# Performance work log

Measured on AMD Instinct MI355X. Metric: run time of the kernel, lower is better.

## Reference

```python
import jax, jax.numpy as jnp
import numpy as np

BN_EPS = 1e-5

def _vq(x, embed):
    # x: (..., dim), embed: (dim, K). Nearest-codeword lookup with straight-through.
    dim = x.shape[-1]
    flat = x.reshape(-1, dim)
    dist = (flat * flat).sum(1, keepdims=True) - 2.0 * (flat @ embed) + (embed * embed).sum(0, keepdims=True)
    ids = jnp.argmin(dist, axis=1)
    q = jnp.take(embed.T, ids, axis=0).reshape(x.shape)
    diff = jnp.mean((jax.lax.stop_gradient(q) - x) ** 2)
    q = x + jax.lax.stop_gradient(q - x)
    return q, diff

def _weight_quantize(W, embed, in_mem, out_mem):
    # W: (out_f, in_f). Group W.T into (out_g, in_g, in_mem*out_mem) blocks,
    # VQ each block, scatter back to (out_f, in_f). Matches torch chunk/stack loops.
    out_f, in_f = W.shape
    in_g, out_g = in_f // in_mem, out_f // out_mem
    g = W.T.reshape(in_g, in_mem, out_g, out_mem).transpose(2, 0, 1, 3).reshape(out_g, in_g, in_mem * out_mem)
    q, diff = _vq(g, embed)
    qW = q.reshape(out_g, in_g, in_mem, out_mem).transpose(0, 3, 1, 2).reshape(out_f, in_f)
    return qW, diff

def _bn(x, gamma, beta):
    # training-mode BatchNorm1d: biased batch variance
    mu = x.mean(axis=0)
    var = ((x - mu) ** 2).mean(axis=0)
    return (x - mu) * jax.lax.rsqrt(var + BN_EPS) * gamma + beta


def setup_inputs() -> dict:
    key = jax.random.key(0)
    ks = jax.random.split(key, 8)
    B, D_IN, H, D_OUT, K = 65536, 784, 512, 10, 512
    s = 0.05
    return {
        "x": jax.random.normal(ks[0], (B, D_IN), jnp.float32),
        "W1": jax.random.normal(ks[1], (H, D_IN), jnp.float32) * s,
        "b1": jnp.zeros((H,), jnp.float32),
        "gamma1": jnp.ones((H,), jnp.float32),
        "beta1": jnp.zeros((H,), jnp.float32),
        "E1": jax.random.normal(ks[2], (28, K), jnp.float32) * s,  # dim = in_mem(7)*out_mem(4)
        "W2": jax.random.normal(ks[3], (H, H), jnp.float32) * s,
        "b2": jnp.zeros((H,), jnp.float32),
        "E2": jax.random.normal(ks[4], (16, K), jnp.float32) * s,  # dim = in_mem(16)*out_mem(1)
        "W3": jax.random.normal(ks[5], (D_OUT, H), jnp.float32) * s,
        "b3": jnp.zeros((D_OUT,), jnp.float32),
    }


def reference(x, W1, b1, gamma1, beta1, E1, W2, b2, E2, W3, b3):
    qW1, diff1 = _weight_quantize(W1, E1, 7, 4)
    h = jax.nn.relu(x @ qW1.T + b1)
    qW2, diff2 = _weight_quantize(W2, E2, 16, 1)
    h = jax.nn.relu(_bn(h, gamma1, beta1) @ qW2.T + b2)
    out = h @ W3.T + b3
    return out, diff1 + diff2
```

## Files before the change

kernel.cpp:

```cpp
#include <hip/hip_runtime.h>
#include <stdint.h>

#define BATCH   65536
#define D_IN    784
#define KP      800
#define HDIM    512
#define D_OUT   10
#define NCODE   512

typedef _Float16 f16;
typedef _Float16 f16x8 __attribute__((ext_vector_type(8)));
typedef float    f32x4 __attribute__((ext_vector_type(4)));

__device__ __forceinline__ void gld_lds16(const void* g, void* l) {
  __builtin_amdgcn_global_load_lds((const __attribute__((address_space(1))) void*)g,
                                   (__attribute__((address_space(3))) void*)l, 16, 0, 0);
}

__global__ void k_convert_x(const float* __restrict__ x, f16* __restrict__ xh) {
  int t = blockIdx.x * 256 + threadIdx.x;
  int r = t / 100;
  int c = (t - r * 100) * 8;
  f16x8 o;
  if (c < D_IN) {
    const float4 a = *(const float4*)(x + (size_t)r * D_IN + c);
    const float4 b = *(const float4*)(x + (size_t)r * D_IN + c + 4);
    o[0]=(f16)a.x; o[1]=(f16)a.y; o[2]=(f16)a.z; o[3]=(f16)a.w;
    o[4]=(f16)b.x; o[5]=(f16)b.y; o[6]=(f16)b.z; o[7]=(f16)b.w;
  } else {
    #pragma unroll
    for (int j = 0; j < 8; ++j) o[j] = (f16)0.f;
  }
  *(f16x8*)(xh + (size_t)r * KP + c) = o;
}

__global__ void k_vq1(const float* __restrict__ W1, const float* __restrict__ E1,
                      f16* __restrict__ qW1, float* __restrict__ diffacc) {
  #pragma clang fp contract(off)
  __shared__ float E1s[28 * NCODE];
  __shared__ float Ts[NCODE];
  for (int i = threadIdx.x; i < 28 * NCODE; i += 256) E1s[i] = E1[i];
  __syncthreads();
  for (int k = threadIdx.x; k < NCODE; k += 256) {
    float e0 = E1s[k];
    float t = e0 * e0;
    for (int j = 1; j < 28; ++j) {
      float e = E1s[j * NCODE + k];
      float ee = e * e;
      t = t + ee;
    }
    Ts[k] = t;
  }
  __syncthreads();
  const int wid = threadIdx.x >> 6, lane = threadIdx.x & 63;
  const int bid = blockIdx.x * 4 + wid;
  const int og = bid / 112, ig = bid % 112;
  float v[28], vv[28];
  #pragma unroll
  for (int j = 0; j < 28; ++j) {
    int om = j & 3, im = j >> 2;
    v[j] = W1[(og * 4 + om) * D_IN + ig * 7 + im];
    vv[j] = v[j] * v[j];
  }
  float r[8];
  #pragma unroll
  for (int j = 0; j < 8; ++j) r[j] = vv[j];
  #pragma unroll
  for (int j = 0; j < 8; ++j) r[j] = r[j] + vv[8 + j];
  #pragma unroll
  for (int j = 0; j < 8; ++j) r[j] = r[j] + vv[16 + j];
  float s = ((r[0] + r[1]) + (r[2] + r[3])) + ((r[4] + r[5]) + (r[6] + r[7]));
  s = s + vv[24]; s = s + vv[25]; s = s + vv[26]; s = s + vv[27];

  float bestd = 1e30f; int bestk = 0x7fffffff;
  for (int t = 0; t < 8; ++t) {
    int k = t * 64 + lane;
    float dot = 0.f;
    #pragma unroll
    for (int j = 0; j < 28; ++j) dot = __builtin_fmaf(v[j], E1s[j * NCODE + k], dot);
    float d = (s - 2.0f * dot) + Ts[k];
    if (d < bestd || (d == bestd && k < bestk)) { bestd = d; bestk = k; }
  }
  for (int off = 32; off; off >>= 1) {
    float d2 = __shfl_down(bestd, off, 64);
    int   k2 = __shfl_down(bestk, off, 64);
    if (d2 < bestd || (d2 == bestd && k2 < bestk)) { bestd = d2; bestk = k2; }
  }
  int kstar = __shfl(bestk, 0, 64);
  float sq = 0.f;
  if (lane < 28) {
    int om = lane & 3, im = lane >> 2;
    float q = E1s[lane * NCODE + kstar];
    qW1[(size_t)(og * 4 + om) * KP + ig * 7 + im] = (f16)q;
    float dd = q - v[lane]; sq = dd * dd;
  }
  for (int off = 32; off; off >>= 1) sq += __shfl_down(sq, off, 64);
  if (lane == 0) atomicAdd(&diffacc[bid & 127], sq);
}

__global__ void k_vq2(const float* __restrict__ W2, const float* __restrict__ E2,
                      f16* __restrict__ qW2, float* __restrict__ diffacc) {
  #pragma clang fp contract(off)
  __shared__ float E2s[16 * NCODE];
  __shared__ float Ts[NCODE];
  for (int i = threadIdx.x; i < 16 * NCODE; i += 256) E2s[i] = E2[i];
  __syncthreads();
  for (int k = threadIdx.x; k < NCODE; k += 256) {
    float e0 = E2s[k];
    float t = e0 * e0;
    for (int j = 1; j < 16; ++j) {
      float e = E2s[j * NCODE + k];
      float ee = e * e;
      t = t + ee;
    }
    Ts[k] = t;
  }
  __syncthreads();
  const int wid = threadIdx.x >> 6, lane = threadIdx.x & 63;
  const int bid = blockIdx.x * 4 + wid;
  const int og = bid >> 5, ig = bid & 31;
  float v[16], vv[16];
  #pragma unroll
  for (int j = 0; j < 16; ++j) {
    v[j] = W2[og * HDIM + ig * 16 + j];
    vv[j] = v[j] * v[j];
  }
  float r[8];
  #pragma unroll
  for (int j = 0; j < 8; ++j) r[j] = vv[j];
  #pragma unroll
  for (int j = 0; j < 8; ++j) r[j] = r[j] + vv[8 + j];
  float s = ((r[0] + r[1]) + (r[2] + r[3])) + ((r[4] + r[5]) + (r[6] + r[7]));

  float bestd = 1e30f; int bestk = 0x7fffffff;
  for (int t = 0; t < 8; ++t) {
    int k = t * 64 + lane;
    float dot = 0.f;
    #pragma unroll
    for (int j = 0; j < 16; ++j) dot = __builtin_fmaf(v[j], E2s[j * NCODE + k], dot);
    float d = (s - 2.0f * dot) + Ts[k];
    if (d < bestd || (d == bestd && k < bestk)) { bestd = d; bestk = k; }
  }
  for (int off = 32; off; off >>= 1) {
    float d2 = __shfl_down(bestd, off, 64);
    int   k2 = __shfl_down(bestk, off, 64);
    if (d2 < bestd || (d2 == bestd && k2 < bestk)) { bestd = d2; bestk = k2; }
  }
  int kstar = __shfl(bestk, 0, 64);
  float sq = 0.f;
  if (lane < 16) {
    float q = E2s[lane * NCODE + kstar];
    qW2[(size_t)og * HDIM + ig * 16 + lane] = (f16)q;
    float dd = q - v[lane]; sq = dd * dd;
  }
  for (int off = 32; off; off >>= 1) sq += __shfl_down(sq, off, 64);
  if (lane == 0) atomicAdd(&diffacc[bid & 127], sq);
}

__global__ void k_gemm(const f16* __restrict__ A, const f16* __restrict__ Bw,
                       const float* __restrict__ bias, f16* __restrict__ C,
                       int K, int lda, int ldb) {
  __shared__ __align__(16) f16 As[128 * 32];
  __shared__ __align__(16) f16 Bs[128 * 32];
  const int tid = threadIdx.x;
  const int bn = blockIdx.x & 3;
  const int bm = blockIdx.x >> 2;
  const int lane = tid & 63, wid = tid >> 6;
  const int waveM = wid & 1, waveN = wid >> 1;
  const int l15 = lane & 15, quad = lane >> 4;

  const int c0 = tid, c1 = tid + 256;
  const f16* gA0 = A + (size_t)(bm * 128 + (c0 >> 2)) * lda + (c0 & 3) * 8;
  const f16* gA1 = A + (size_t)(bm * 128 + (c1 >> 2)) * lda + (c1 & 3) * 8;
  const f16* gB0 = Bw + (size_t)(bn * 128 + (c0 >> 2)) * ldb + (c0 & 3) * 8;
  const f16* gB1 = Bw + (size_t)(bn * 128 + (c1 >> 2)) * ldb + (c1 & 3) * 8;
  f16* lA0 = As + c0 * 8; f16* lA1 = As + c1 * 8;
  f16* lB0 = Bs + c0 * 8; f16* lB1 = Bs + c1 * 8;

  f32x4 acc[4][4];
  #pragma unroll
  for (int i = 0; i < 4; ++i)
    #pragma unroll
    for (int j = 0; j < 4; ++j) acc[i][j] = (f32x4){0.f, 0.f, 0.f, 0.f};

  const int aoff = (waveM * 64 + l15) * 32 + quad * 8;
  const int boff = (waveN * 64 + l15) * 32 + quad * 8;

  for (int k0 = 0; k0 < K; k0 += 32) {
    gld_lds16(gA0 + k0, lA0);
    gld_lds16(gA1 + k0, lA1);
    gld_lds16(gB0 + k0, lB0);
    gld_lds16(gB1 + k0, lB1);
    __syncthreads();
    f16x8 af[4], bf[4];
    #pragma unroll
    for (int i = 0; i < 4; ++i) af[i] = *(const f16x8*)(As + aoff + i * 16 * 32);
    #pragma unroll
    for (int j = 0; j < 4; ++j) bf[j] = *(const f16x8*)(Bs + boff + j * 16 * 32);
    #pragma unroll
    for (int i = 0; i < 4; ++i)
      #pragma unroll
      for (int j = 0; j < 4; ++j)
        acc[i][j] = __builtin_amdgcn_mfma_f32_16x16x32_f16(af[i], bf[j], acc[i][j], 0, 0, 0);
    __syncthreads();
  }
  const int colbase = bn * 128 + waveN * 64 + l15;
  float bcol[4];
  #pragma unroll
  for (int j = 0; j < 4; ++j) bcol[j] = bias[colbase + j * 16];
  const int rowbase = bm * 128 + waveM * 64 + quad * 4;
  #pragma unroll
  for (int i = 0; i < 4; ++i)
    #pragma unroll
    for (int r = 0; r < 4; ++r) {
      f16* crow = C + (size_t)(rowbase + i * 16 + r) * HDIM + colbase;
      #pragma unroll
      for (int j = 0; j < 4; ++j) {
        float v = acc[i][j][r] + bcol[j];
        crow[j * 16] = (f16)(v > 0.f ? v : 0.f);
      }
    }
}

__global__ void k_stats(const f16* __restrict__ h, float* __restrict__ acc) {
  const int c = threadIdx.x;
  size_t base = (size_t)blockIdx.x * 128 * HDIM + c;
  float s = 0.f, s2 = 0.f;
  for (int i = 0; i < 128; ++i) {
    float v = (float)h[base + (size_t)i * HDIM];
    s += v; s2 += v * v;
  }
  atomicAdd(&acc[256 + c], s);
  atomicAdd(&acc[768 + c], s2);
}

__global__ void k_bnprep(const float* __restrict__ acc, const float* __restrict__ gamma,
                         const float* __restrict__ beta, float* __restrict__ ab,
                         const float* __restrict__ W3, f16* __restrict__ W3h,
                         float* __restrict__ diff_out) {
  const int c = threadIdx.x;
  const float inv = 1.f / 65536.f;
  float mu = acc[256 + c] * inv;
  float msq = acc[768 + c] * inv;
  float var = msq - mu * mu;
  float a = gamma[c] / sqrtf(var + 1e-5f);
  ab[c] = a;
  ab[512 + c] = beta[c] - mu * a;
  #pragma unroll
  for (int o = 0; o < 16; ++o)
    W3h[o * HDIM + c] = (o < D_OUT) ? (f16)W3[o * HDIM + c] : (f16)0.f;
  if (c == 0) {
    float s1 = 0.f, s2 = 0.f;
    for (int i = 0; i < 128; ++i) { s1 += acc[i]; s2 += acc[128 + i]; }
    diff_out[0] = s1 * (1.f / 401408.f) + s2 * (1.f / 262144.f);
  }
}

__global__ void k_bnapply(f16* __restrict__ h, const float* __restrict__ ab) {
  size_t t = (size_t)blockIdx.x * 256 + threadIdx.x;
  int cg = (int)(t & 63) * 8;
  f16x8 v = *(f16x8*)(h + t * 8);
  #pragma unroll
  for (int j = 0; j < 8; ++j) {
    float f = (float)v[j] * ab[cg + j] + ab[512 + cg + j];
    v[j] = (f16)f;
  }
  *(f16x8*)(h + t * 8) = v;
}

__global__ void k_final(const f16* __restrict__ h2, const f16* __restrict__ W3h,
                        const float* __restrict__ b3, float* __restrict__ out) {
  const int tid = threadIdx.x;
  const int wid = tid >> 6, lane = tid & 63;
  const int l15 = lane & 15, quad = lane >> 4;
  const int r0 = (blockIdx.x * 4 + wid) * 16;
  f32x4 acc = (f32x4){0.f, 0.f, 0.f, 0.f};
  const f16* arow = h2 + (size_t)(r0 + l15) * HDIM + quad * 8;
  const f16* brow = W3h + (size_t)l15 * HDIM + quad * 8;
  #pragma unroll
  for (int k0 = 0; k0 < HDIM; k0 += 32) {
    f16x8 a = *(const f16x8*)(arow + k0);
    f16x8 b = *(const f16x8*)(brow + k0);
    acc = __builtin_amdgcn_mfma_f32_16x16x32_f16(a, b, acc, 0, 0, 0);
  }
  if (l15 < D_OUT) {
    float bias = b3[l15];
    #pragma unroll
    for (int r = 0; r < 4; ++r)
      out[(size_t)(r0 + quad * 4 + r) * D_OUT + l15] = acc[r] + bias;
  }
}

extern "C" void kernel_launch(void* const* d_in, const int* in_sizes, int n_in,
                              void* d_out, int out_size, void* d_ws, size_t ws_size,
                              hipStream_t stream) {
  const float* x     = (const float*)d_in[0];
  const float* W1    = (const float*)d_in[1];
  const float* b1    = (const float*)d_in[2];
  const float* gamma = (const float*)d_in[3];
  const float* beta  = (const float*)d_in[4];
  const float* E1    = (const float*)d_in[5];
  const float* W2    = (const float*)d_in[6];
  const float* b2    = (const float*)d_in[7];
  const float* E2    = (const float*)d_in[8];
  const float* W3    = (const float*)d_in[9];
  const float* b3    = (const float*)d_in[10];
  float* out = (float*)d_out;

  char* ws = (char*)d_ws;
  float* accum = (float*)ws;
  f16* qW1h = (f16*)(ws + 8192);
  f16* qW2h = (f16*)(ws + 827392);
  f16* W3h  = (f16*)(ws + 1351680);
  float* ab = (float*)(ws + 1368064);
  f16* xh   = (f16*)(ws + 1372160);
  f16* h    = (f16*)(ws + 106229760);
  f16* h2   = xh;

  hipMemsetAsync(ws, 0, 827392, stream);
  k_convert_x<<<25600, 256, 0, stream>>>(x, xh);
  k_vq1<<<3584, 256, 0, stream>>>(W1, E1, qW1h, accum);
  k_vq2<<<4096, 256, 0, stream>>>(W2, E2, qW2h, accum + 128);
  k_gemm<<<2048, 256, 0, stream>>>(xh, qW1h, b1, h, KP, KP, KP);
  k_stats<<<512, 512, 0, stream>>>(h, accum);
  k_bnprep<<<1, 512, 0, stream>>>(accum, gamma, beta, ab, W3, W3h, out + (size_t)BATCH * D_OUT);
  k_bnapply<<<16384, 256, 0, stream>>>(h, ab);
  k_gemm<<<2048, 256, 0, stream>>>(h, qW2h, b2, h2, HDIM, HDIM, HDIM);
  k_final<<<1024, 256, 0, stream>>>(h2, W3h, b3, out);
}
```

Measured before the change: 630.9 us.

## Fuse BN stats into GEMM1, fold BN into W2, fuse final layer

Column sum and sum-of-squares for batch norm are now computed in the first GEMM's epilogue, using LDS and atomics. This replaces a separate stats pass over h. The BN scale and shift are folded into qW2 and a new bias by a small kernel, which removes the elementwise normalize pass. The third (10-wide) layer runs in the second GEMM's epilogue from an LDS-staged tile, with partial sums across N-blocks combined by atomics into a zeroed output. This cuts several full passes over the large activation tensor, at the cost of output atomics and folding BN into f16 weights, which may change rounding.

```diff
diff --git a/kernel.cpp b/kernel.cpp
--- a/kernel.cpp
+++ b/kernel.cpp
@@ -7,6 +7,7 @@
 #define HDIM    512
 #define D_OUT   10
 #define NCODE   512
+#define HT_LD   136
 
 typedef _Float16 f16;
 typedef _Float16 f16x8 __attribute__((ext_vector_type(8)));
@@ -157,11 +158,14 @@
   if (lane == 0) atomicAdd(&diffacc[bid & 127], sq);
 }
 
-__global__ void k_gemm(const f16* __restrict__ A, const f16* __restrict__ Bw,
-                       const float* __restrict__ bias, f16* __restrict__ C,
-                       int K, int lda, int ldb) {
-  __shared__ __align__(16) f16 As[128 * 32];
-  __shared__ __align__(16) f16 Bs[128 * 32];
+__global__ void k_gemm1(const f16* __restrict__ A, const f16* __restrict__ Bw,
+                        const float* __restrict__ bias, f16* __restrict__ C,
+                        float* __restrict__ statacc) {
+  __shared__ __align__(16) char lds_all[HT_LD * 128 * 2];
+  __shared__ float cls[128], cls2[128];
+  f16* As = (f16*)lds_all;
+  f16* Bs = (f16*)(lds_all + 8192);
+  f16* ht = (f16*)lds_all;
   const int tid = threadIdx.x;
   const int bn = blockIdx.x & 3;
   const int bm = blockIdx.x >> 2;
@@ -169,11 +173,13 @@
   const int waveM = wid & 1, waveN = wid >> 1;
   const int l15 = lane & 15, quad = lane >> 4;
 
+  if (tid < 128) cls[tid] = 0.f; else cls2[tid - 128] = 0.f;
+
   const int c0 = tid, c1 = tid + 256;
-  const f16* gA0 = A + (size_t)(bm * 128 + (c0 >> 2)) * lda + (c0 & 3) * 8;
-  const f16* gA1 = A + (size_t)(bm * 128 + (c1 >> 2)) * lda + (c1 & 3) * 8;
-  const f16* gB0 = Bw + (size_t)(bn * 128 + (c0 >> 2)) * ldb + (c0 & 3) * 8;
-  const f16* gB1 = Bw + (size_t)(bn * 128 + (c1 >> 2)) * ldb + (c1 & 3) * 8;
+  const f16* gA0 = A + (size_t)(bm * 128 + (c0 >> 2)) * KP + (c0 & 3) * 8;
+  const f16* gA1 = A + (size_t)(bm * 128 + (c1 >> 2)) * KP + (c1 & 3) * 8;
+  const f16* gB0 = Bw + (size_t)(bn * 128 + (c0 >> 2)) * KP + (c0 & 3) * 8;
+  const f16* gB1 = Bw + (size_t)(bn * 128 + (c1 >> 2)) * KP + (c1 & 3) * 8;
   f16* lA0 = As + c0 * 8; f16* lA1 = As + c1 * 8;
   f16* lB0 = Bs + c0 * 8; f16* lB1 = Bs + c1 * 8;
 
@@ -186,7 +192,7 @@
   const int aoff = (waveM * 64 + l15) * 32 + quad * 8;
   const int boff = (waveN * 64 + l15) * 32 + quad * 8;
 
-  for (int k0 = 0; k0 < K; k0 += 32) {
+  for (int k0 = 0; k0 < KP; k0 += 32) {
     gld_lds16(gA0 + k0, lA0);
     gld_lds16(gA1 + k0, lA1);
     gld_lds16(gB0 + k0, lB0);
@@ -208,30 +214,43 @@
   float bcol[4];
   #pragma unroll
   for (int j = 0; j < 4; ++j) bcol[j] = bias[colbase + j * 16];
-  const int rowbase = bm * 128 + waveM * 64 + quad * 4;
+  float cs[4] = {0.f,0.f,0.f,0.f}, cs2[4] = {0.f,0.f,0.f,0.f};
   #pragma unroll
   for (int i = 0; i < 4; ++i)
     #pragma unroll
-    for (int r = 0; r < 4; ++r) {
-      f16* crow = C + (size_t)(rowbase + i * 16 + r) * HDIM + colbase;
+    for (int r2 = 0; r2 < 4; ++r2) {
+      int rloc = waveM * 64 + quad * 4 + i * 16 + r2;
       #pragma unroll
       for (int j = 0; j < 4; ++j) {
-        float v = acc[i][j][r] + bcol[j];
-        crow[j * 16] = (f16)(v > 0.f ? v : 0.f);
+        float v = acc[i][j][r2] + bcol[j];
+        v = v > 0.f ? v : 0.f;
+        ht[rloc * HT_LD + waveN * 64 + j * 16 + l15] = (f16)v;
+        cs[j] += v; cs2[j] += v * v;
       }
     }
-}
-
-__global__ void k_stats(const f16* __restrict__ h, float* __restrict__ acc) {
-  const int c = threadIdx.x;
-  size_t base = (size_t)blockIdx.x * 128 * HDIM + c;
-  float s = 0.f, s2 = 0.f;
-  for (int i = 0; i < 128; ++i) {
-    float v = (float)h[base + (size_t)i * HDIM];
-    s += v; s2 += v * v;
-  }
-  atomicAdd(&acc[256 + c], s);
-  atomicAdd(&acc[768 + c], s2);
+  #pragma unroll
+  for (int j = 0; j < 4; ++j) {
+    cs[j]  += __shfl_xor(cs[j], 16, 64);  cs[j]  += __shfl_xor(cs[j], 32, 64);
+    cs2[j] += __shfl_xor(cs2[j], 16, 64); cs2[j] += __shfl_xor(cs2[j], 32, 64);
+  }
+  if (quad == 0) {
+    #pragma unroll
+    for (int j = 0; j < 4; ++j) {
+      atomicAdd(&cls[waveN * 64 + j * 16 + l15], cs[j]);
+      atomicAdd(&cls2[waveN * 64 + j * 16 + l15], cs2[j]);
+    }
+  }
+  __syncthreads();
+  if (tid < 128) atomicAdd(&statacc[256 + bn * 128 + tid], cls[tid]);
+  else           atomicAdd(&statacc[768 + bn * 128 + (tid - 128)], cls2[tid - 128]);
+  {
+    const int rloc = tid >> 1, half = tid & 1;
+    f16* crow = C + (size_t)(bm * 128 + rloc) * HDIM + bn * 128 + half * 64;
+    const f16* srow = ht + rloc * HT_LD + half * 64;
+    #pragma unroll
+    for (int j = 0; j < 8; ++j)
+      *(f16x8*)(crow + j * 8) = *(const f16x8*)(srow + j * 8);
+  }
 }
 
 __global__ void k_bnprep(const float* __restrict__ acc, const float* __restrict__ gamma,
@@ -256,38 +275,109 @@
   }
 }
 
-__global__ void k_bnapply(f16* __restrict__ h, const float* __restrict__ ab) {
-  size_t t = (size_t)blockIdx.x * 256 + threadIdx.x;
-  int cg = (int)(t & 63) * 8;
-  f16x8 v = *(f16x8*)(h + t * 8);
-  #pragma unroll
-  for (int j = 0; j < 8; ++j) {
-    float f = (float)v[j] * ab[cg + j] + ab[512 + cg + j];
-    v[j] = (f16)f;
-  }
-  *(f16x8*)(h + t * 8) = v;
-}
-
-__global__ void k_final(const f16* __restrict__ h2, const f16* __restrict__ W3h,
-                        const float* __restrict__ b3, float* __restrict__ out) {
+__global__ void k_bnfold(f16* __restrict__ qW2, const float* __restrict__ ab,
+                         const float* __restrict__ b2, float* __restrict__ bias2) {
+  __shared__ float red[256];
+  const int n = blockIdx.x, t = threadIdx.x;
+  float partial = 0.f;
+  #pragma unroll
+  for (int kk = 0; kk < 2; ++kk) {
+    int k = t + kk * 256;
+    float w = (float)qW2[n * HDIM + k];
+    partial += ab[512 + k] * w;
+    qW2[n * HDIM + k] = (f16)(ab[k] * w);
+  }
+  red[t] = partial; __syncthreads();
+  for (int s = 128; s > 0; s >>= 1) { if (t < s) red[t] += red[t + s]; __syncthreads(); }
+  if (t == 0) bias2[n] = b2[n] + red[0];
+}
+
+__global__ void k_gemm2f(const f16* __restrict__ A, const f16* __restrict__ Bw,
+                         const float* __restrict__ bias2, const f16* __restrict__ W3h,
+                         const float* __restrict__ b3, float* __restrict__ out) {
+  __shared__ __align__(16) char lds_all[HT_LD * 128 * 2];
+  f16* As = (f16*)lds_all;
+  f16* Bs = (f16*)(lds_all + 8192);
+  f16* ht = (f16*)lds_all;
   const int tid = threadIdx.x;
-  const int wid = tid >> 6, lane = tid & 63;
+  const int bn = blockIdx.x & 3;
+  const int bm = blockIdx.x >> 2;
+  const int lane = tid & 63, wid = tid >> 6;
+  const int waveM = wid & 1, waveN = wid >> 1;
   const int l15 = lane & 15, quad = lane >> 4;
-  const int r0 = (blockIdx.x * 4 + wid) * 16;
-  f32x4 acc = (f32x4){0.f, 0.f, 0.f, 0.f};
-  const f16* arow = h2 + (size_t)(r0 + l15) * HDIM + quad * 8;
-  const f16* brow = W3h + (size_t)l15 * HDIM + quad * 8;
-  #pragma unroll
+
+  const int c0 = tid, c1 = tid + 256;
+  const f16* gA0 = A + (size_t)(bm * 128 + (c0 >> 2)) * HDIM + (c0 & 3) * 8;
+  const f16* gA1 = A + (size_t)(bm * 128 + (c1 >> 2)) * HDIM + (c1 & 3) * 8;
+  const f16* gB0 = Bw + (size_t)(bn * 128 + (c0 >> 2)) * HDIM + (c0 & 3) * 8;
+  const f16* gB1 = Bw + (size_t)(bn * 128 + (c1 >> 2)) * HDIM + (c1 & 3) * 8;
+  f16* lA0 = As + c0 * 8; f16* lA1 = As + c1 * 8;
+  f16* lB0 = Bs + c0 * 8; f16* lB1 = Bs + c1 * 8;
+
+  f32x4 acc[4][4];
+  #pragma unroll
+  for (int i = 0; i < 4; ++i)
+    #pragma unroll
+    for (int j = 0; j < 4; ++j) acc[i][j] = (f32x4){0.f, 0.f, 0.f, 0.f};
+
+  const int aoff = (waveM * 64 + l15) * 32 + quad * 8;
+  const int boff = (waveN * 64 + l15) * 32 + quad * 8;
+
   for (int k0 = 0; k0 < HDIM; k0 += 32) {
-    f16x8 a = *(const f16x8*)(arow + k0);
-    f16x8 b = *(const f16x8*)(brow + k0);
-    acc = __builtin_amdgcn_mfma_f32_16x16x32_f16(a, b, acc, 0, 0, 0);
+    gld_lds16(gA0 + k0, lA0);
+    gld_lds16(gA1 + k0, lA1);
+    gld_lds16(gB0 + k0, lB0);
+    gld_lds16(gB1 + k0, lB1);
+    __syncthreads();
+    f16x8 af[4], bf[4];
+    #pragma unroll
+    for (int i = 0; i < 4; ++i) af[i] = *(const f16x8*)(As + aoff + i * 16 * 32);
+    #pragma unroll
+    for (int j = 0; j < 4; ++j) bf[j] = *(const f16x8*)(Bs + boff + j * 16 * 32);
+    #pragma unroll
+    for (int i = 0; i < 4; ++i)
+      #pragma unroll
+      for (int j = 0; j < 4; ++j)
+        acc[i][j] = __builtin_amdgcn_mfma_f32_16x16x32_f16(af[i], bf[j], acc[i][j], 0, 0, 0);
+    __syncthreads();
+  }
+  const int colbase = bn * 128 + waveN * 64 + l15;
+  float bcol[4];
+  #pragma unroll
+  for (int j = 0; j < 4; ++j) bcol[j] = bias2[colbase + j * 16];
+  #pragma unroll
+  for (int i = 0; i < 4; ++i)
+    #pragma unroll
+    for (int r2 = 0; r2 < 4; ++r2) {
+      int rloc = waveM * 64 + quad * 4 + i * 16 + r2;
+      #pragma unroll
+      for (int j = 0; j < 4; ++j) {
+        float v = acc[i][j][r2] + bcol[j];
+        v = v > 0.f ? v : 0.f;
+        ht[rloc * HT_LD + waveN * 64 + j * 16 + l15] = (f16)v;
+      }
+    }
+  __syncthreads();
+  f32x4 oacc[2];
+  oacc[0] = (f32x4){0.f,0.f,0.f,0.f}; oacc[1] = (f32x4){0.f,0.f,0.f,0.f};
+  #pragma unroll
+  for (int ks = 0; ks < 4; ++ks) {
+    f16x8 bfr = *(const f16x8*)(W3h + l15 * HDIM + bn * 128 + ks * 32 + quad * 8);
+    #pragma unroll
+    for (int i2 = 0; i2 < 2; ++i2) {
+      f16x8 afr = *(const f16x8*)(ht + (wid * 32 + i2 * 16 + l15) * HT_LD + ks * 32 + quad * 8);
+      oacc[i2] = __builtin_amdgcn_mfma_f32_16x16x32_f16(afr, bfr, oacc[i2], 0, 0, 0);
+    }
   }
   if (l15 < D_OUT) {
-    float bias = b3[l15];
-    #pragma unroll
-    for (int r = 0; r < 4; ++r)
-      out[(size_t)(r0 + quad * 4 + r) * D_OUT + l15] = acc[r] + bias;
+    float badd = (bn == 0) ? b3[l15] : 0.f;
+    #pragma unroll
+    for (int i2 = 0; i2 < 2; ++i2)
+      #pragma unroll
+      for (int r2 = 0; r2 < 4; ++r2) {
+        int row = bm * 128 + wid * 32 + i2 * 16 + quad * 4 + r2;
+        atomicAdd(&out[(size_t)row * D_OUT + l15], oacc[i2][r2] + badd);
+      }
   }
 }
 
@@ -313,18 +403,17 @@
   f16* qW2h = (f16*)(ws + 827392);
   f16* W3h  = (f16*)(ws + 1351680);
   float* ab = (float*)(ws + 1368064);
-  f16* xh   = (f16*)(ws + 1372160);
-  f16* h    = (f16*)(ws + 106229760);
-  f16* h2   = xh;
+  float* bias2 = (float*)(ws + 1372160);
+  f16* xh   = (f16*)(ws + 1376256);
+  f16* h    = (f16*)(ws + 106233856);
 
   hipMemsetAsync(ws, 0, 827392, stream);
+  hipMemsetAsync(d_out, 0, (size_t)out_size * 4, stream);
   k_convert_x<<<25600, 256, 0, stream>>>(x, xh);
   k_vq1<<<3584, 256, 0, stream>>>(W1, E1, qW1h, accum);
   k_vq2<<<4096, 256, 0, stream>>>(W2, E2, qW2h, accum + 128);
-  k_gemm<<<2048, 256, 0, stream>>>(xh, qW1h, b1, h, KP, KP, KP);
-  k_stats<<<512, 512, 0, stream>>>(h, accum);
+  k_gemm1<<<2048, 256, 0, stream>>>(xh, qW1h, b1, h, accum);
   k_bnprep<<<1, 512, 0, stream>>>(accum, gamma, beta, ab, W3, W3h, out + (size_t)BATCH * D_OUT);
-  k_bnapply<<<16384, 256, 0, stream>>>(h, ab);
-  k_gemm<<<2048, 256, 0, stream>>>(h, qW2h, b2, h2, HDIM, HDIM, HDIM);
-  k_final<<<1024, 256, 0, stream>>>(h2, W3h, b3, out);
-}
+  k_bnfold<<<512, 256, 0, stream>>>(qW2h, ab, b2, bias2);
+  k_gemm2f<<<2048, 256, 0, stream>>>(h, qW2h, bias2, W3h, b3, out);
+}
```

New measurement: 601.8 us. 4.6% less time.
